# Kernel optimization log

Measured on AMD Instinct MI355X. Metric: run time of the kernel, lower is better.

## Reference

```python
import jax, jax.numpy as jnp
import numpy as np

EPS = 1e-6
NUM_HEADS = 16

def _ln(x):
    m = jnp.mean(x, -1, keepdims=True)
    v = jnp.mean((x - m) ** 2, -1, keepdims=True)
    return (x - m) * jax.lax.rsqrt(v + EPS)

def _rms(x, w):
    return x * jax.lax.rsqrt(jnp.mean(x * x, -1, keepdims=True) + EPS) * w

def _to_mha(t):
    B, S, D = t.shape
    return t.reshape(B, S, NUM_HEADS, D // NUM_HEADS).transpose(0, 2, 1, 3)

def _rope(t, freqs):
    # t: [B,H,T,Hd], freqs: [T, Hd//2, 2] (cos, sin)
    B, H, T, Hd = t.shape
    tr = t.reshape(B, H, T, Hd // 2, 2)
    cos, sin = freqs[..., 0], freqs[..., 1]
    r = tr[..., 0] * cos - tr[..., 1] * sin
    i = tr[..., 0] * sin + tr[..., 1] * cos
    return jnp.stack([r, i], -1).reshape(B, H, T, Hd)

def _pre(h, qk_w, qn, kn, v_w, v_b):
    qk = h @ qk_w.T                      # [B,S,2D], no bias (c_qk bias=False)
    q, k = jnp.split(qk, 2, -1)
    q = _rms(_to_mha(q), qn)             # per-head RMSNorm
    k = _rms(_to_mha(k), kn)
    v = _to_mha(h @ v_w.T + v_b)
    return q, k, v

def _post(x, a, pw, pb, w1, b1, w3, b3, w2, b2):
    x = x + a @ pw.T + pb                # residual + c_proj
    h = _ln(x)
    m = (jax.nn.silu(h @ w1.T + b1) * (h @ w3.T + b3)) @ w2.T + b2  # SwiGLU
    return x + m

def _forward(x, c, freqs, px_qk_w, px_qn, px_kn, px_v_w, px_v_b,
             pc_qk_w, pc_qn, pc_kn, pc_v_w, pc_v_b,
             p1_proj_w, p1_proj_b, p1_w1, p1_b1, p1_w3, p1_b3, p1_w2, p1_b2,
             p2_proj_w, p2_proj_b, p2_w1, p2_b1, p2_w3, p2_b3, p2_w2, p2_b2):
    x_ln, c_ln = _ln(x), _ln(c)
    qc, kc, vc = _pre(c_ln, pc_qk_w, pc_qn, pc_kn, pc_v_w, pc_v_b)
    qx, kx, vx = _pre(x_ln, px_qk_w, px_qn, px_kn, px_v_w, px_v_b)
    q = jnp.concatenate([qc, qx], 2)     # [B,H,T,Hd], T = S+L
    k = jnp.concatenate([kc, kx], 2)
    v = jnp.concatenate([vc, vx], 2)
    q = _rope(q, freqs)
    k = _rope(k, freqs)
    Hd = q.shape[-1]
    scores = jnp.einsum('bhqd,bhkd->bhqk', q, k) / jnp.sqrt(jnp.float32(Hd))
    T = scores.shape[-1]
    causal = jnp.tril(jnp.ones((T, T), bool))
    scores = jnp.where(causal, scores, jnp.finfo(scores.dtype).min)
    p = jax.nn.softmax(scores, -1)
    y = jnp.einsum('bhqk,bhkd->bhqd', p, v)
    B, D = x.shape[0], x.shape[-1]
    y = y.transpose(0, 2, 1, 3).reshape(B, -1, D)  # [B,T,D]
    S = c.shape[1]
    y_c, y_x = y[:, :S], y[:, S:]
    x_out = _post(x, y_x, p1_proj_w, p1_proj_b, p1_w1, p1_b1, p1_w3, p1_b3, p1_w2, p1_b2)
    c_out = _post(c, y_c, p2_proj_w, p2_proj_b, p2_w1, p2_b1, p2_w3, p2_b3, p2_w2, p2_b2)
    return x_out, c_out

def setup_inputs() -> dict:
    B, L, S, D, H, FF = 1, 1536, 512, 1024, 16, 4096
    Hd, T = D // H, L + S
    key = jax.random.key(0)
    ks = iter(jax.random.split(key, 40))
    def rn(shape, s=0.02):
        return (jax.random.normal(next(ks), shape, jnp.float32) * s)
    pos = jnp.arange(T, dtype=jnp.float32)
    inv = 1.0 / (10000.0 ** (jnp.arange(0, Hd, 2, dtype=jnp.float32) / Hd))
    ang = pos[:, None] * inv[None, :]
    freqs = jnp.stack([jnp.cos(ang), jnp.sin(ang)], -1)  # [T, Hd//2, 2]
    inp = {
        'x': jax.random.normal(next(ks), (B, L, D), jnp.float32),
        'c': jax.random.normal(next(ks), (B, S, D), jnp.float32),
        'freqs': freqs,
        'px_qk_w': rn((2 * D, D)), 'px_qn': jnp.ones((Hd,)), 'px_kn': jnp.ones((Hd,)),
        'px_v_w': rn((D, D)), 'px_v_b': rn((D,)),
        'pc_qk_w': rn((2 * D, D)), 'pc_qn': jnp.ones((Hd,)), 'pc_kn': jnp.ones((Hd,)),
        'pc_v_w': rn((D, D)), 'pc_v_b': rn((D,)),
    }
    for pfx in ('p1', 'p2'):
        inp[pfx + '_proj_w'] = rn((D, D)); inp[pfx + '_proj_b'] = rn((D,))
        inp[pfx + '_w1'] = rn((FF, D)); inp[pfx + '_b1'] = rn((FF,))
        inp[pfx + '_w3'] = rn((FF, D)); inp[pfx + '_b3'] = rn((FF,))
        inp[pfx + '_w2'] = rn((D, FF)); inp[pfx + '_b2'] = rn((D,))
    return inp

def reference(x, c, freqs, px_qk_w, px_qn, px_kn, px_v_w, px_v_b,
              pc_qk_w, pc_qn, pc_kn, pc_v_w, pc_v_b,
              p1_proj_w, p1_proj_b, p1_w1, p1_b1, p1_w3, p1_b3, p1_w2, p1_b2,
              p2_proj_w, p2_proj_b, p2_w1, p2_b1, p2_w3, p2_b3, p2_w2, p2_b2):
    return _forward(x, c, freqs, px_qk_w, px_qn, px_kn, px_v_w, px_v_b,
                    pc_qk_w, pc_qn, pc_kn, pc_v_w, pc_v_b,
                    p1_proj_w, p1_proj_b, p1_w1, p1_b1, p1_w3, p1_b3, p1_w2, p1_b2,
                    p2_proj_w, p2_proj_b, p2_w1, p2_b1, p2_w3, p2_b3, p2_w2, p2_b2)
```

## Files before the change

kernel.cpp:

```cpp
#include <hip/hip_runtime.h>

typedef __attribute__((ext_vector_type(8))) short short8;
typedef __attribute__((ext_vector_type(4))) float floatx4;

__device__ __forceinline__ float bf2f(unsigned short u) {
  union { unsigned int i; float f; } v; v.i = ((unsigned int)u) << 16; return v.f;
}
__device__ __forceinline__ unsigned short f2bf(float f) {
  union { float f; unsigned int i; } v; v.f = f;
  unsigned int x = v.i + 0x7fffu + ((v.i >> 16) & 1u);
  return (unsigned short)(x >> 16);
}
__device__ __forceinline__ float loadE(const void* p, size_t i, int f) {
  return f ? ((const float*)p)[i] : bf2f(((const unsigned short*)p)[i]);
}
__device__ __forceinline__ uint4 packbf(float4 a, float4 b) {
  union { unsigned short u[8]; uint4 v; } p;
  p.u[0] = f2bf(a.x); p.u[1] = f2bf(a.y); p.u[2] = f2bf(a.z); p.u[3] = f2bf(a.w);
  p.u[4] = f2bf(b.x); p.u[5] = f2bf(b.y); p.u[6] = f2bf(b.z); p.u[7] = f2bf(b.w);
  return p.v;
}

__device__ __forceinline__ void gl16(const unsigned short* g, unsigned short* l) {
  __builtin_amdgcn_global_load_lds(
      (const __attribute__((address_space(1))) void*)g,
      (__attribute__((address_space(3))) void*)l, 16, 0, 0);
}

__global__ void detect_kernel(const unsigned int* __restrict__ probe, int* __restrict__ flag) {
  if (threadIdx.x == 0 && blockIdx.x == 0) *flag = (probe[0] == 0x3F800000u) ? 1 : 0;
}

struct CArgs {
  const void* in[12];
  unsigned short* out[12];
  unsigned int cum[12];
};
__global__ __launch_bounds__(256) void convw_kernel(CArgs a, int total_chunks,
                                                    const int* __restrict__ flagp) {
  const int flag = *flagp;
  for (int c = blockIdx.x * 256 + threadIdx.x; c < total_chunks; c += gridDim.x * 256) {
    int s = 0;
    while (c >= (int)a.cum[s]) ++s;
    unsigned int base = s ? a.cum[s - 1] : 0u;
    size_t e = (size_t)(c - base) * 8;
    if (flag) {
      const float* in = (const float*)a.in[s] + e;
      float4 v0 = *(const float4*)in;
      float4 v1 = *(const float4*)(in + 4);
      *(uint4*)(a.out[s] + e) = packbf(v0, v1);
    } else {
      *(uint4*)(a.out[s] + e) = *(const uint4*)((const unsigned short*)a.in[s] + e);
    }
  }
}

__global__ __launch_bounds__(256) void zero_kernel(void* __restrict__ out, int out_elems,
                                                   const int* __restrict__ flagp) {
  int limit = (*flagp) ? (out_elems >> 2) : (out_elems >> 3);
  int i = blockIdx.x * 256 + threadIdx.x;
  if (i < limit) ((uint4*)out)[i] = make_uint4(0, 0, 0, 0);
}

__global__ __launch_bounds__(256) void reduce_kernel(const float* __restrict__ part,
                                                     const unsigned short* __restrict__ mid,
                                                     const void* __restrict__ b1,
                                                     const void* __restrict__ b2,
                                                     float* __restrict__ out,
                                                     const int* __restrict__ flagp) {
  if (!*flagp) return;
  const size_t TD = 2097152, LD = (size_t)1536 * 1024, SD = (size_t)512 * 1024;
  size_t i = ((size_t)blockIdx.x * 256 + threadIdx.x) * 4;
  if (i >= TD) return;
  float4 v  = *(const float4*)(part + i);
  float4 v1 = *(const float4*)(part + TD + i);
  float4 v2 = *(const float4*)(part + 2 * TD + i);
  float4 v3 = *(const float4*)(part + 3 * TD + i);
  v.x += v1.x + v2.x + v3.x;
  v.y += v1.y + v2.y + v3.y;
  v.z += v1.z + v2.z + v3.z;
  v.w += v1.w + v2.w + v3.w;
  int col = (int)(i & 1023);
  const float* bias = (const float*)((i < LD) ? b1 : b2);
  size_t ri = (i < LD) ? (SD + i) : (i - LD);
  v.x += bias[col + 0] + bf2f(mid[ri + 0]);
  v.y += bias[col + 1] + bf2f(mid[ri + 1]);
  v.z += bias[col + 2] + bf2f(mid[ri + 2]);
  v.w += bias[col + 3] + bf2f(mid[ri + 3]);
  *(float4*)(out + i) = v;
}

__global__ __launch_bounds__(256) void ln_ext_kernel(const void* __restrict__ cin,
                                                     const void* __restrict__ xin,
                                                     unsigned short* __restrict__ out,
                                                     const int* __restrict__ flagp) {
  const int D = 1024, S = 512;
  const int flag = *flagp;
  int row = blockIdx.x;
  const void* src = (row < S) ? cin : xin;
  size_t rb = (size_t)(row < S ? row : row - S) * D;
  int base = threadIdx.x * 4;
  float x0 = loadE(src, rb + base + 0, flag);
  float x1 = loadE(src, rb + base + 1, flag);
  float x2 = loadE(src, rb + base + 2, flag);
  float x3 = loadE(src, rb + base + 3, flag);
  float s1 = x0 + x1 + x2 + x3;
  float s2 = x0 * x0 + x1 * x1 + x2 * x2 + x3 * x3;
  for (int off = 32; off; off >>= 1) {
    s1 += __shfl_down(s1, off, 64);
    s2 += __shfl_down(s2, off, 64);
  }
  __shared__ float red[8];
  int wid = threadIdx.x >> 6;
  if ((threadIdx.x & 63) == 0) { red[wid] = s1; red[4 + wid] = s2; }
  __syncthreads();
  s1 = red[0] + red[1] + red[2] + red[3];
  s2 = red[4] + red[5] + red[6] + red[7];
  float mean = s1 * (1.0f / D);
  float var = s2 * (1.0f / D) - mean * mean;
  float inv = rsqrtf(var + 1e-6f);
  unsigned short* dst = out + (size_t)row * D + base;
  dst[0] = f2bf((x0 - mean) * inv);
  dst[1] = f2bf((x1 - mean) * inv);
  dst[2] = f2bf((x2 - mean) * inv);
  dst[3] = f2bf((x3 - mean) * inv);
}

__global__ __launch_bounds__(256) void ln_mid_kernel(const unsigned short* __restrict__ in,
                                                     unsigned short* __restrict__ outc,
                                                     unsigned short* __restrict__ outx) {
  const int D = 1024, S = 512;
  int row = blockIdx.x;
  const unsigned short* src = in + (size_t)row * D;
  int base = threadIdx.x * 4;
  float x0 = bf2f(src[base + 0]);
  float x1 = bf2f(src[base + 1]);
  float x2 = bf2f(src[base + 2]);
  float x3 = bf2f(src[base + 3]);
  float s1 = x0 + x1 + x2 + x3;
  float s2 = x0 * x0 + x1 * x1 + x2 * x2 + x3 * x3;
  for (int off = 32; off; off >>= 1) {
    s1 += __shfl_down(s1, off, 64);
    s2 += __shfl_down(s2, off, 64);
  }
  __shared__ float red[8];
  int wid = threadIdx.x >> 6;
  if ((threadIdx.x & 63) == 0) { red[wid] = s1; red[4 + wid] = s2; }
  __syncthreads();
  s1 = red[0] + red[1] + red[2] + red[3];
  s2 = red[4] + red[5] + red[6] + red[7];
  float mean = s1 * (1.0f / D);
  float var = s2 * (1.0f / D) - mean * mean;
  float inv = rsqrtf(var + 1e-6f);
  unsigned short* dst = (row < S ? outc + (size_t)row * D : outx + (size_t)(row - S) * D) + base;
  dst[0] = f2bf((x0 - mean) * inv);
  dst[1] = f2bf((x1 - mean) * inv);
  dst[2] = f2bf((x2 - mean) * inv);
  dst[3] = f2bf((x3 - mean) * inv);
}

struct GArgs {
  const unsigned short* A[4];
  const void* B[4];
  const void* bias[4];
  const void* res[4];
  void* C[4];
  unsigned long long oo[4];
  int mcum[4];
  int N[4];
  int K;
  int nd;
  float* part;
};

#define BAR() asm volatile("s_waitcnt lgkmcnt(0)\n\ts_barrier" ::: "memory")
#define FBAR() asm volatile("s_waitcnt vmcnt(0) lgkmcnt(0)\n\ts_barrier" ::: "memory")

template <int RES_MODE, int OUT_MODE, int SPLITK, int BBF16>
__global__ __launch_bounds__(256) void gemm_kernel(GArgs g, const int* __restrict__ flagp) {
  const int flag = *flagp;
  int by = blockIdx.y;
  int d = 0;
  while (d < g.nd - 1 && by >= g.mcum[d]) ++d;
  int mbase = (d == 0) ? 0 : g.mcum[d - 1];
  const int m0 = (by - mbase) * 128;
  const int N = g.N[d];
  const int n0 = blockIdx.x * 128;
  if (n0 >= N) return;
  const int K = g.K;
  int kbeg = 0, kend = K;
  if (SPLITK > 1) {
    if (!flag) {
      if (blockIdx.z != 0) return;
    } else {
      int kl = K / SPLITK;
      kbeg = blockIdx.z * kl;
      kend = kbeg + kl;
    }
  }
  const int nt = (kend - kbeg) >> 5;

  constexpr int BSTRIDE = BBF16 ? 4096 : 5120;
  __shared__ __align__(16) unsigned short sA[2 * BSTRIDE];
  __shared__ __align__(16) unsigned short sB[2 * BSTRIDE];

  const int tid = threadIdx.x;
  const int lane = tid & 63;
  const int wave = tid >> 6;
  const int wm = (wave >> 1) * 64, wn = (wave & 1) * 64;
  const int srow = tid >> 2;
  const int scol = BBF16 ? ((((tid & 3) ^ ((tid >> 3) & 3))) * 8) : ((tid & 3) * 8);
  const unsigned short* Ag0 = g.A[d] + (size_t)(m0 + srow) * K + kbeg + scol;
  const unsigned short* Ag1 = Ag0 + (size_t)64 * K;
  const unsigned short* Bh0 = (const unsigned short*)g.B[d] + (size_t)(n0 + srow) * K + kbeg + scol;
  const unsigned short* Bh1 = Bh0 + (size_t)64 * K;

  const int fr = lane & 15;
  const int rdo = BBF16 ? ((((lane >> 4) ^ ((fr >> 1) & 3))) * 8) : ((lane >> 4) * 8);
  constexpr int PITCH = BBF16 ? 32 : 40;
  floatx4 acc[4][4] = {};
  auto compute = [&](const unsigned short* as, const unsigned short* bs) {
    short8 af[4], bfr[4];
    #pragma unroll
    for (int i = 0; i < 4; ++i) {
      af[i]  = *(const short8*)(as + (wm + i * 16 + fr) * PITCH + rdo);
      bfr[i] = *(const short8*)(bs + (wn + i * 16 + fr) * PITCH + rdo);
    }
    #pragma unroll
    for (int mi = 0; mi < 4; ++mi)
      #pragma unroll
      for (int ni = 0; ni < 4; ++ni)
        acc[mi][ni] = __builtin_amdgcn_mfma_f32_16x16x32_bf16(af[mi], bfr[ni], acc[mi][ni], 0, 0, 0);
  };

  if (BBF16) {
    unsigned short* lA0 = sA + wave * 512;
    unsigned short* lA1 = lA0 + 2048;
    unsigned short* lB0 = sB + wave * 512;
    unsigned short* lB1 = lB0 + 2048;
    auto stage = [&](int buf, int kk) {
      int bo = buf * 4096;
      gl16(Ag0 + kk, lA0 + bo);
      gl16(Ag1 + kk, lA1 + bo);
      gl16(Bh0 + kk, lB0 + bo);
      gl16(Bh1 + kk, lB1 + bo);
    };
    stage(0, 0);
    FBAR();
    for (int t = 0; t < nt; ++t) {
      if (t + 1 < nt) stage((t + 1) & 1, (t + 1) * 32);
      compute(sA + (t & 1) * 4096, sB + (t & 1) * 4096);
      if (t + 1 < nt) FBAR();
    }
  } else {
    const float* Bf0 = (const float*)g.B[d] + (size_t)(n0 + srow) * K + kbeg + scol;
    const float* Bf1 = Bf0 + (size_t)64 * K;
    const int wo0 = srow * 40 + scol;
    const int wo1 = wo0 + 64 * 40;
    uint4 ra0, ra1, rb0, rb1;
    auto load_tile = [&](int kk) {
      ra0 = *(const uint4*)(Ag0 + kk);
      ra1 = *(const uint4*)(Ag1 + kk);
      if (!flag) {
        rb0 = *(const uint4*)(Bh0 + kk);
        rb1 = *(const uint4*)(Bh1 + kk);
      } else {
        float4 x0 = *(const float4*)(Bf0 + kk), x1 = *(const float4*)(Bf0 + kk + 4);
        float4 y0 = *(const float4*)(Bf1 + kk), y1 = *(const float4*)(Bf1 + kk + 4);
        rb0 = packbf(x0, x1);
        rb1 = packbf(y0, y1);
      }
    };
    auto store_tile = [&](int buf) {
      unsigned short* sa = sA + buf * 5120;
      unsigned short* sb = sB + buf * 5120;
      *(uint4*)(sa + wo0) = ra0;
      *(uint4*)(sa + wo1) = ra1;
      *(uint4*)(sb + wo0) = rb0;
      *(uint4*)(sb + wo1) = rb1;
    };
    load_tile(0);
    store_tile(0);
    if (nt > 1) load_tile(32);
    BAR();
    for (int t = 0; t < nt; ++t) {
      if (t + 1 < nt) {
        store_tile((t + 1) & 1);
        if (t + 2 < nt) load_tile((t + 2) * 32);
      }
      compute(sA + (t & 1) * 5120, sB + (t & 1) * 5120);
      if (t + 1 < nt) BAR();
    }
  }

  const void* bias = g.bias[d];
  const void* res = g.res[d];
  void* C = g.C[d];
  const size_t oo = g.oo[d];
  const bool first = (SPLITK <= 1) || (blockIdx.z == 0) || !flag;
  const bool rawpart = (OUT_MODE == 3) && (flag != 0);
  #pragma unroll
  for (int mi = 0; mi < 4; ++mi)
    #pragma unroll
    for (int ni = 0; ni < 4; ++ni)
      #pragma unroll
      for (int r = 0; r < 4; ++r) {
        int row = m0 + wm + mi * 16 + (lane >> 4) * 4 + r;
        int col = n0 + wn + ni * 16 + (lane & 15);
        float val = acc[mi][ni][r];
        size_t off = (size_t)row * N + col;
        if (first && !rawpart) {
          if (bias) val += loadE(bias, (size_t)col, flag);
          if (RES_MODE == 1) val += loadE(res, off, flag);
          if (RES_MODE == 3) {
            float h1v = bf2f(((const unsigned short*)res)[off]);
            val = (h1v / (1.0f + __expf(-h1v))) * val;
          }
          if (RES_MODE == 4) val += bf2f(((const unsigned short*)res)[off]);
        }
        if (OUT_MODE == 0) {
          ((unsigned short*)C)[off] = f2bf(val);
        } else if (OUT_MODE == 3) {
          if (flag) g.part[(size_t)blockIdx.z * 2097152 + oo + off] = val;
          else      ((unsigned short*)C)[oo + off] = f2bf(val);
        } else {
          if (flag) {
            if (SPLITK > 1) atomicAdd((float*)C + oo + off, val);
            else            ((float*)C)[oo + off] = val;
          } else {
            ((unsigned short*)C)[oo + off] = f2bf(val);
          }
        }
      }
}

__global__ __launch_bounds__(256) void rmsrope_kernel(
    unsigned short* __restrict__ qk,
    const void* __restrict__ qn_c, const void* __restrict__ kn_c,
    const void* __restrict__ qn_x, const void* __restrict__ kn_x,
    const void* __restrict__ freqs, const int* __restrict__ flagp) {
  const int flag = *flagp;
  int t = blockIdx.x;
  int h = blockIdx.y * 4 + (threadIdx.x >> 6);
  int d = threadIdx.x & 63;
  unsigned short* qrow = qk + (size_t)t * 2048 + h * 64;
  unsigned short* krow = qrow + 1024;
  float q = bf2f(qrow[d]), k = bf2f(krow[d]);
  float qs = q * q, ks = k * k;
  for (int off = 32; off; off >>= 1) {
    qs += __shfl_xor(qs, off, 64);
    ks += __shfl_xor(ks, off, 64);
  }
  const void* qn = (t < 512) ? qn_c : qn_x;
  const void* kn = (t < 512) ? kn_c : kn_x;
  q = q * rsqrtf(qs * (1.0f / 64.0f) + 1e-6f) * loadE(qn, d, flag);
  k = k * rsqrtf(ks * (1.0f / 64.0f) + 1e-6f) * loadE(kn, d, flag);
  int j = d >> 1;
  float cv = loadE(freqs, (size_t)(t * 32 + j) * 2 + 0, flag);
  float sv = loadE(freqs, (size_t)(t * 32 + j) * 2 + 1, flag);
  float qo = __shfl_xor(q, 1, 64);
  float ko = __shfl_xor(k, 1, 64);
  float qn2, kn2;
  if ((d & 1) == 0) { qn2 = q * cv - qo * sv; kn2 = k * cv - ko * sv; }
  else              { qn2 = qo * sv + q * cv; kn2 = ko * sv + k * cv; }
  qrow[d] = f2bf(qn2);
  krow[d] = f2bf(kn2);
}

__global__ __launch_bounds__(256) void attn_kernel(const unsigned short* __restrict__ qk,
                                                   const unsigned short* __restrict__ v,
                                                   unsigned short* __restrict__ y) {
  int id = blockIdx.x;
  int blk = (id & 256) ? (31 - (id & 31)) : (id & 31);
  int h = (id >> 5) & 15;
  int wv = threadIdx.x >> 6;
  int lane = threadIdx.x & 63;
  int qbase = blk * 64 + wv * 16;

  __shared__ __align__(16) unsigned short Ks[64 * 72];
  __shared__ __align__(16) unsigned short Vt[64 * 64];
  __shared__ __align__(16) unsigned short ps[4][16 * 72];

  short8 qa[2];
  {
    int m = lane & 15, dj = (lane >> 4) * 8;
    const unsigned short* qp = qk + (size_t)(qbase + m) * 2048 + h * 64 + dj;
    qa[0] = *(const short8*)(qp);
    qa[1] = *(const short8*)(qp + 32);
  }
  floatx4 o[4] = {};
  float mrow[4] = {-1e30f, -1e30f, -1e30f, -1e30f};
  float lrow[4] = {0.f, 0.f, 0.f, 0.f};
  int ntiles = blk + 1;
  for (int tile = 0; tile < ntiles; ++tile) {
    int j0 = tile * 64;
    __syncthreads();
    for (int c2 = threadIdx.x; c2 < 512; c2 += 256) {
      int key = c2 >> 3, d0 = (c2 & 7) * 8;
      *(short8*)(Ks + key * 72 + d0) =
          *(const short8*)(qk + (size_t)(j0 + key) * 2048 + 1024 + h * 64 + d0);
      short8 vv = *(const short8*)(v + (size_t)(j0 + key) * 1024 + h * 64 + d0);
      int bphys = ((key >> 3) ^ (d0 >> 3)) * 8 + (key & 7);
      #pragma unroll
      for (int jj = 0; jj < 8; ++jj)
        Vt[(d0 + jj) * 64 + bphys] = ((const unsigned short*)&vv)[jj];
    }
    __syncthreads();
    floatx4 sacc[4];
    #pragma unroll
    for (int kg = 0; kg < 4; ++kg) {
      floatx4 z = {0.f, 0.f, 0.f, 0.f};
      #pragma unroll
      for (int kc = 0; kc < 2; ++kc) {
        short8 kb = *(const short8*)(Ks + (kg * 16 + (lane & 15)) * 72 + kc * 32 + (lane >> 4) * 8);
        z = __builtin_amdgcn_mfma_f32_16x16x32_bf16(qa[kc], kb, z, 0, 0, 0);
      }
      sacc[kg] = z;
    }
    #pragma unroll
    for (int kg = 0; kg < 4; ++kg)
      #pragma unroll
      for (int r = 0; r < 4; ++r) {
        int key_g = j0 + kg * 16 + (lane & 15);
        int q_g = qbase + (lane >> 4) * 4 + r;
        float s = sacc[kg][r] * 0.125f;
        sacc[kg][r] = (key_g <= q_g) ? s : -1e30f;
      }
    #pragma unroll
    for (int r = 0; r < 4; ++r) {
      float mx = fmaxf(fmaxf(sacc[0][r], sacc[1][r]), fmaxf(sacc[2][r], sacc[3][r]));
      mx = fmaxf(mx, __shfl_xor(mx, 1, 64));
      mx = fmaxf(mx, __shfl_xor(mx, 2, 64));
      mx = fmaxf(mx, __shfl_xor(mx, 4, 64));
      mx = fmaxf(mx, __shfl_xor(mx, 8, 64));
      float mnew = fmaxf(mrow[r], mx);
      float al = __expf(mrow[r] - mnew);
      mrow[r] = mnew;
      float sum = 0.f;
      #pragma unroll
      for (int kg = 0; kg < 4; ++kg) {
        float p = __expf(sacc[kg][r] - mnew);
        sacc[kg][r] = p;
        sum += p;
      }
      sum += __shfl_xor(sum, 1, 64);
      sum += __shfl_xor(sum, 2, 64);
      sum += __shfl_xor(sum, 4, 64);
      sum += __shfl_xor(sum, 8, 64);
      lrow[r] = lrow[r] * al + sum;
      #pragma unroll
      for (int ni = 0; ni < 4; ++ni) o[ni][r] *= al;
    }
    unsigned short* pw = ps[wv];
    #pragma unroll
    for (int kg = 0; kg < 4; ++kg)
      #pragma unroll
      for (int r = 0; r < 4; ++r)
        pw[((lane >> 4) * 4 + r) * 72 + kg * 16 + (lane & 15)] = f2bf(sacc[kg][r]);
    asm volatile("s_waitcnt lgkmcnt(0)" ::: "memory");
    short8 pa[2];
    pa[0] = *(const short8*)(pw + (lane & 15) * 72 + (lane >> 4) * 8);
    pa[1] = *(const short8*)(pw + (lane & 15) * 72 + 32 + (lane >> 4) * 8);
    #pragma unroll
    for (int ni = 0; ni < 4; ++ni) {
      floatx4 z = o[ni];
      int dd = ni * 16 + (lane & 15);
      #pragma unroll
      for (int kc = 0; kc < 2; ++kc) {
        int bphys = (kc * 4 + (lane >> 4)) ^ (dd >> 3);
        short8 vb = *(const short8*)(Vt + dd * 64 + bphys * 8);
        z = __builtin_amdgcn_mfma_f32_16x16x32_bf16(pa[kc], vb, z, 0, 0, 0);
      }
      o[ni] = z;
    }
  }
  #pragma unroll
  for (int ni = 0; ni < 4; ++ni)
    #pragma unroll
    for (int r = 0; r < 4; ++r) {
      int q = qbase + (lane >> 4) * 4 + r;
      int dd = ni * 16 + (lane & 15);
      y[(size_t)q * 1024 + h * 64 + dd] = f2bf(o[ni][r] / lrow[r]);
    }
}

extern "C" void kernel_launch(void* const* d_in, const int* in_sizes, int n_in,
                              void* d_out, int out_size, void* d_ws, size_t ws_size,
                              hipStream_t stream) {
  const int L = 1536, S = 512, D = 1024, T = 2048, FF = 4096;
  const void* x        = d_in[0];
  const void* c        = d_in[1];
  const void* freqs    = d_in[2];
  const void* px_qk_w  = d_in[3];
  const void* px_qn    = d_in[4];
  const void* px_kn    = d_in[5];
  const void* px_v_w   = d_in[6];
  const void* px_v_b   = d_in[7];
  const void* pc_qk_w  = d_in[8];
  const void* pc_qn    = d_in[9];
  const void* pc_kn    = d_in[10];
  const void* pc_v_w   = d_in[11];
  const void* pc_v_b   = d_in[12];
  const void* p1_proj_w = d_in[13];
  const void* p1_proj_b = d_in[14];
  const void* p1_w1 = d_in[15];
  const void* p1_b1 = d_in[16];
  const void* p1_w3 = d_in[17];
  const void* p1_b3 = d_in[18];
  const void* p1_w2 = d_in[19];
  const void* p1_b2 = d_in[20];
  const void* p2_proj_w = d_in[21];
  const void* p2_proj_b = d_in[22];
  const void* p2_w1 = d_in[23];
  const void* p2_b1 = d_in[24];
  const void* p2_w3 = d_in[25];
  const void* p2_b3 = d_in[26];
  const void* p2_w2 = d_in[27];
  const void* p2_b2 = d_in[28];

  char* ws = (char*)d_ws;
  unsigned short* hln     = (unsigned short*)(ws);
  unsigned short* ybuf    = (unsigned short*)(ws);
  unsigned short* h1c     = (unsigned short*)(ws);
  unsigned short* qkbuf   = (unsigned short*)(ws + ((size_t)4  << 20));
  unsigned short* h1x     = (unsigned short*)(ws + ((size_t)4  << 20));
  unsigned short* vbuf    = (unsigned short*)(ws + ((size_t)12 << 20));
  unsigned short* mid     = (unsigned short*)(ws + ((size_t)16 << 20));
  unsigned short* midln_c = (unsigned short*)(ws + ((size_t)20 << 20));
  int*            flag    = (int*)(ws + ((size_t)21 << 20));
  unsigned short* midln_x = (unsigned short*)d_out;
  unsigned short* hlnx    = hln + (size_t)S * D;

  const bool conv = ws_size >= ((size_t)90 << 20);
  unsigned short* wbf = (unsigned short*)(ws + ((size_t)24 << 20));
  unsigned short* b_qk_c = wbf + 0;
  unsigned short* b_qk_x = wbf + 2097152;
  unsigned short* b_v_c  = wbf + 4194304;
  unsigned short* b_v_x  = wbf + 5242880;
  unsigned short* b_pj1  = wbf + 6291456;
  unsigned short* b_pj2  = wbf + 7340032;
  unsigned short* b_w1p1 = wbf + 8388608;
  unsigned short* b_w1p2 = wbf + 12582912;
  unsigned short* b_w3p1 = wbf + 16777216;
  unsigned short* b_w3p2 = wbf + 20971520;
  unsigned short* b_w2p1 = wbf + 25165824;
  unsigned short* b_w2p2 = wbf + 29360128;
  float* part = (float*)(ws + ((size_t)40 << 20));

  detect_kernel<<<1, 64, 0, stream>>>((const unsigned int*)px_qn, flag);

  if (conv) {
    CArgs ca;
    const void* ins[12]   = {pc_qk_w, px_qk_w, pc_v_w, px_v_w, p1_proj_w, p2_proj_w,
                             p1_w1, p2_w1, p1_w3, p2_w3, p1_w2, p2_w2};
    unsigned short* os[12] = {b_qk_c, b_qk_x, b_v_c, b_v_x, b_pj1, b_pj2,
                              b_w1p1, b_w1p2, b_w3p1, b_w3p2, b_w2p1, b_w2p2};
    unsigned int cnt[12]  = {262144, 262144, 131072, 131072, 131072, 131072,
                             524288, 524288, 524288, 524288, 524288, 524288};
    unsigned int cum = 0;
    for (int i = 0; i < 12; ++i) { ca.in[i] = ins[i]; ca.out[i] = os[i]; cum += cnt[i]; ca.cum[i] = cum; }
    convw_kernel<<<2048, 256, 0, stream>>>(ca, (int)cum, flag);
  }

  ln_ext_kernel<<<T, 256, 0, stream>>>(c, x, hln, flag);

  {
    GArgs g = {};
    g.A[0] = hln;  g.bias[0] = nullptr; g.C[0] = qkbuf;                    g.mcum[0] = 4;  g.N[0] = 2048;
    g.A[1] = hlnx; g.bias[1] = nullptr; g.C[1] = qkbuf + (size_t)S * 2048; g.mcum[1] = 16; g.N[1] = 2048;
    g.A[2] = hln;  g.bias[2] = pc_v_b;  g.C[2] = vbuf;                     g.mcum[2] = 20; g.N[2] = 1024;
    g.A[3] = hlnx; g.bias[3] = px_v_b;  g.C[3] = vbuf + (size_t)S * D;     g.mcum[3] = 32; g.N[3] = 1024;
    g.K = 1024; g.nd = 4;
    if (conv) {
      g.B[0] = b_qk_c; g.B[1] = b_qk_x; g.B[2] = b_v_c; g.B[3] = b_v_x;
      gemm_kernel<0, 0, 1, 1><<<dim3(16, 32), 256, 0, stream>>>(g, flag);
    } else {
      g.B[0] = pc_qk_w; g.B[1] = px_qk_w; g.B[2] = pc_v_w; g.B[3] = px_v_w;
      gemm_kernel<0, 0, 1, 0><<<dim3(16, 32), 256, 0, stream>>>(g, flag);
    }
  }
  rmsrope_kernel<<<dim3(T, 4), 256, 0, stream>>>(qkbuf, pc_qn, pc_kn, px_qn, px_kn, freqs, flag);
  attn_kernel<<<512, 256, 0, stream>>>(qkbuf, vbuf, ybuf);

  {
    GArgs g = {};
    g.A[0] = ybuf;                  g.bias[0] = p2_proj_b; g.res[0] = c; g.C[0] = mid;                  g.mcum[0] = 4;  g.N[0] = 1024;
    g.A[1] = ybuf + (size_t)S * D;  g.bias[1] = p1_proj_b; g.res[1] = x; g.C[1] = mid + (size_t)S * D;  g.mcum[1] = 16; g.N[1] = 1024;
    g.K = 1024; g.nd = 2;
    if (conv) {
      g.B[0] = b_pj2; g.B[1] = b_pj1;
      gemm_kernel<1, 0, 1, 1><<<dim3(8, 16), 256, 0, stream>>>(g, flag);
    } else {
      g.B[0] = p2_proj_w; g.B[1] = p1_proj_w;
      gemm_kernel<1, 0, 1, 0><<<dim3(8, 16), 256, 0, stream>>>(g, flag);
    }
  }
  ln_mid_kernel<<<T, 256, 0, stream>>>(mid, midln_c, midln_x);

  {
    GArgs g = {};
    g.A[0] = midln_x; g.bias[0] = p1_b1; g.C[0] = h1x; g.mcum[0] = 12; g.N[0] = 4096;
    g.A[1] = midln_c; g.bias[1] = p2_b1; g.C[1] = h1c; g.mcum[1] = 16; g.N[1] = 4096;
    g.K = 1024; g.nd = 2;
    if (conv) {
      g.B[0] = b_w1p1; g.B[1] = b_w1p2;
      gemm_kernel<0, 0, 1, 1><<<dim3(32, 16), 256, 0, stream>>>(g, flag);
    } else {
      g.B[0] = p1_w1; g.B[1] = p2_w1;
      gemm_kernel<0, 0, 1, 0><<<dim3(32, 16), 256, 0, stream>>>(g, flag);
    }
  }
  {
    GArgs g = {};
    g.A[0] = midln_x; g.bias[0] = p1_b3; g.res[0] = h1x; g.C[0] = h1x; g.mcum[0] = 12; g.N[0] = 4096;
    g.A[1] = midln_c; g.bias[1] = p2_b3; g.res[1] = h1c; g.C[1] = h1c; g.mcum[1] = 16; g.N[1] = 4096;
    g.K = 1024; g.nd = 2;
    if (conv) {
      g.B[0] = b_w3p1; g.B[1] = b_w3p2;
      gemm_kernel<3, 0, 1, 1><<<dim3(32, 16), 256, 0, stream>>>(g, flag);
    } else {
      g.B[0] = p1_w3; g.B[1] = p2_w3;
      gemm_kernel<3, 0, 1, 0><<<dim3(32, 16), 256, 0, stream>>>(g, flag);
    }
  }
  if (conv) {
    GArgs g = {};
    g.A[0] = h1x; g.bias[0] = p1_b2; g.res[0] = mid + (size_t)S * D; g.C[0] = d_out; g.oo[0] = 0;             g.mcum[0] = 12; g.N[0] = 1024;
    g.A[1] = h1c; g.bias[1] = p2_b2; g.res[1] = mid;                 g.C[1] = d_out; g.oo[1] = (size_t)L * D; g.mcum[1] = 16; g.N[1] = 1024;
    g.K = 4096; g.nd = 2;
    g.part = part;
    g.B[0] = b_w2p1; g.B[1] = b_w2p2;
    gemm_kernel<4, 3, 4, 1><<<dim3(8, 16, 4), 256, 0, stream>>>(g, flag);
    reduce_kernel<<<2048, 256, 0, stream>>>(part, mid, p1_b2, p2_b2, (float*)d_out, flag);
  } else {
    zero_kernel<<<2048, 256, 0, stream>>>(d_out, out_size, flag);
    GArgs g = {};
    g.A[0] = h1x; g.bias[0] = p1_b2; g.res[0] = mid + (size_t)S * D; g.C[0] = d_out; g.oo[0] = 0;             g.mcum[0] = 12; g.N[0] = 1024;
    g.A[1] = h1c; g.bias[1] = p2_b2; g.res[1] = mid;                 g.C[1] = d_out; g.oo[1] = (size_t)L * D; g.mcum[1] = 16; g.N[1] = 1024;
    g.K = 4096; g.nd = 2;
    g.B[0] = p1_w2; g.B[1] = p2_w2;
    gemm_kernel<4, 2, 4, 0><<<dim3(8, 16, 4), 256, 0, stream>>>(g, flag);
  }
}
```

Before: 511.8 us.

## Write V transposed from GEMM epilogue and double-buffer attention K/V via async LDS loads

The QKV GEMM epilogue now writes the V projection transposed ([D, T] layout) with 4-wide packed stores. This lets the attention kernel load V tiles directly instead of transposing them element by element into shared memory. The attention kernel now uses global_load_lds to stage K and V into double-buffered, XOR-swizzled LDS tiles, prefetching the next tile while the current one is computed. The costs are strided transposed stores in the GEMM epilogue and twice the LDS footprint in attention, which may lower occupancy.

```diff
diff --git a/kernel.cpp b/kernel.cpp
--- a/kernel.cpp
+++ b/kernel.cpp
@@ -2,6 +2,7 @@
 
 typedef __attribute__((ext_vector_type(8))) short short8;
 typedef __attribute__((ext_vector_type(4))) float floatx4;
+typedef __attribute__((ext_vector_type(4))) unsigned short ushortx4;
 
 __device__ __forceinline__ float bf2f(unsigned short u) {
   union { unsigned int i; float f; } v; v.i = ((unsigned int)u) << 16; return v.f;
@@ -170,6 +171,7 @@
   int N[4];
   int K;
   int nd;
+  int tmask;
   float* part;
 };
 
@@ -299,39 +301,54 @@
   const size_t oo = g.oo[d];
   const bool first = (SPLITK <= 1) || (blockIdx.z == 0) || !flag;
   const bool rawpart = (OUT_MODE == 3) && (flag != 0);
+  const bool trans = (OUT_MODE == 0) && (((g.tmask) >> d) & 1);
   #pragma unroll
   for (int mi = 0; mi < 4; ++mi)
     #pragma unroll
-    for (int ni = 0; ni < 4; ++ni)
-      #pragma unroll
-      for (int r = 0; r < 4; ++r) {
-        int row = m0 + wm + mi * 16 + (lane >> 4) * 4 + r;
-        int col = n0 + wn + ni * 16 + (lane & 15);
-        float val = acc[mi][ni][r];
-        size_t off = (size_t)row * N + col;
-        if (first && !rawpart) {
-          if (bias) val += loadE(bias, (size_t)col, flag);
-          if (RES_MODE == 1) val += loadE(res, off, flag);
-          if (RES_MODE == 3) {
-            float h1v = bf2f(((const unsigned short*)res)[off]);
-            val = (h1v / (1.0f + __expf(-h1v))) * val;
+    for (int ni = 0; ni < 4; ++ni) {
+      int colb = n0 + wn + ni * 16 + (lane & 15);
+      int rowb = m0 + wm + mi * 16 + (lane >> 4) * 4;
+      if (trans) {
+        ushortx4 o4;
+        #pragma unroll
+        for (int r = 0; r < 4; ++r) {
+          float val = acc[mi][ni][r];
+          if (bias) val += loadE(bias, (size_t)colb, flag);
+          o4[r] = f2bf(val);
+        }
+        *(ushortx4*)((unsigned short*)C + (size_t)colb * 2048 + oo + rowb) = o4;
+      } else {
+        #pragma unroll
+        for (int r = 0; r < 4; ++r) {
+          int row = rowb + r;
+          int col = colb;
+          float val = acc[mi][ni][r];
+          size_t off = (size_t)row * N + col;
+          if (first && !rawpart) {
+            if (bias) val += loadE(bias, (size_t)col, flag);
+            if (RES_MODE == 1) val += loadE(res, off, flag);
+            if (RES_MODE == 3) {
+              float h1v = bf2f(((const unsigned short*)res)[off]);
+              val = (h1v / (1.0f + __expf(-h1v))) * val;
+            }
+            if (RES_MODE == 4) val += bf2f(((const unsigned short*)res)[off]);
           }
-          if (RES_MODE == 4) val += bf2f(((const unsigned short*)res)[off]);
-        }
-        if (OUT_MODE == 0) {
-          ((unsigned short*)C)[off] = f2bf(val);
-        } else if (OUT_MODE == 3) {
-          if (flag) g.part[(size_t)blockIdx.z * 2097152 + oo + off] = val;
-          else      ((unsigned short*)C)[oo + off] = f2bf(val);
-        } else {
-          if (flag) {
-            if (SPLITK > 1) atomicAdd((float*)C + oo + off, val);
-            else            ((float*)C)[oo + off] = val;
+          if (OUT_MODE == 0) {
+            ((unsigned short*)C)[off] = f2bf(val);
+          } else if (OUT_MODE == 3) {
+            if (flag) g.part[(size_t)blockIdx.z * 2097152 + oo + off] = val;
+            else      ((unsigned short*)C)[oo + off] = f2bf(val);
           } else {
-            ((unsigned short*)C)[oo + off] = f2bf(val);
+            if (flag) {
+              if (SPLITK > 1) atomicAdd((float*)C + oo + off, val);
+              else            ((float*)C)[oo + off] = val;
+            } else {
+              ((unsigned short*)C)[oo + off] = f2bf(val);
+            }
           }
         }
       }
+    }
 }
 
 __global__ __launch_bounds__(256) void rmsrope_kernel(
@@ -368,7 +385,7 @@
 }
 
 __global__ __launch_bounds__(256) void attn_kernel(const unsigned short* __restrict__ qk,
-                                                   const unsigned short* __restrict__ v,
+                                                   const unsigned short* __restrict__ vT,
                                                    unsigned short* __restrict__ y) {
   int id = blockIdx.x;
   int blk = (id & 256) ? (31 - (id & 31)) : (id & 31);
@@ -377,9 +394,28 @@
   int lane = threadIdx.x & 63;
   int qbase = blk * 64 + wv * 16;
 
-  __shared__ __align__(16) unsigned short Ks[64 * 72];
-  __shared__ __align__(16) unsigned short Vt[64 * 64];
+  __shared__ __align__(16) unsigned short Ks[2 * 4096];
+  __shared__ __align__(16) unsigned short Vs[2 * 4096];
   __shared__ __align__(16) unsigned short ps[4][16 * 72];
+
+  const int c0 = wv * 64 + lane;
+  const int r0 = c0 >> 3,         k0 = (c0 & 7) ^ (r0 & 7);
+  const int r1 = (c0 + 256) >> 3, k1 = (c0 & 7) ^ (r1 & 7);
+  unsigned short* kd0 = Ks + wv * 512;
+  unsigned short* kd1 = Ks + 2048 + wv * 512;
+  unsigned short* vd0 = Vs + wv * 512;
+  unsigned short* vd1 = Vs + 2048 + wv * 512;
+  const unsigned short* kgp0 = qk + 1024 + h * 64 + k0 * 8 + (size_t)r0 * 2048;
+  const unsigned short* kgp1 = qk + 1024 + h * 64 + k1 * 8 + (size_t)r1 * 2048;
+  const unsigned short* vgp0 = vT + (size_t)(h * 64 + r0) * 2048 + k0 * 8;
+  const unsigned short* vgp1 = vT + (size_t)(h * 64 + r1) * 2048 + k1 * 8;
+  auto stage = [&](int buf, int j0) {
+    int bo = buf * 4096;
+    gl16(kgp0 + (size_t)j0 * 2048, kd0 + bo);
+    gl16(kgp1 + (size_t)j0 * 2048, kd1 + bo);
+    gl16(vgp0 + j0, vd0 + bo);
+    gl16(vgp1 + j0, vd1 + bo);
+  };
 
   short8 qa[2];
   {
@@ -392,27 +428,23 @@
   float mrow[4] = {-1e30f, -1e30f, -1e30f, -1e30f};
   float lrow[4] = {0.f, 0.f, 0.f, 0.f};
   int ntiles = blk + 1;
+
+  stage(0, 0);
+  FBAR();
   for (int tile = 0; tile < ntiles; ++tile) {
     int j0 = tile * 64;
-    __syncthreads();
-    for (int c2 = threadIdx.x; c2 < 512; c2 += 256) {
-      int key = c2 >> 3, d0 = (c2 & 7) * 8;
-      *(short8*)(Ks + key * 72 + d0) =
-          *(const short8*)(qk + (size_t)(j0 + key) * 2048 + 1024 + h * 64 + d0);
-      short8 vv = *(const short8*)(v + (size_t)(j0 + key) * 1024 + h * 64 + d0);
-      int bphys = ((key >> 3) ^ (d0 >> 3)) * 8 + (key & 7);
-      #pragma unroll
-      for (int jj = 0; jj < 8; ++jj)
-        Vt[(d0 + jj) * 64 + bphys] = ((const unsigned short*)&vv)[jj];
-    }
-    __syncthreads();
+    if (tile + 1 < ntiles) stage((tile + 1) & 1, j0 + 64);
+    const unsigned short* Kb = Ks + (tile & 1) * 4096;
+    const unsigned short* Vb = Vs + (tile & 1) * 4096;
     floatx4 sacc[4];
     #pragma unroll
     for (int kg = 0; kg < 4; ++kg) {
       floatx4 z = {0.f, 0.f, 0.f, 0.f};
       #pragma unroll
       for (int kc = 0; kc < 2; ++kc) {
-        short8 kb = *(const short8*)(Ks + (kg * 16 + (lane & 15)) * 72 + kc * 32 + (lane >> 4) * 8);
+        int kr = kg * 16 + (lane & 15);
+        int p = (kc * 4 + (lane >> 4)) ^ (kr & 7);
+        short8 kb = *(const short8*)(Kb + kr * 64 + p * 8);
         z = __builtin_amdgcn_mfma_f32_16x16x32_bf16(qa[kc], kb, z, 0, 0, 0);
       }
       sacc[kg] = z;
@@ -467,12 +499,13 @@
       int dd = ni * 16 + (lane & 15);
       #pragma unroll
       for (int kc = 0; kc < 2; ++kc) {
-        int bphys = (kc * 4 + (lane >> 4)) ^ (dd >> 3);
-        short8 vb = *(const short8*)(Vt + dd * 64 + bphys * 8);
+        int p = (kc * 4 + (lane >> 4)) ^ (dd & 7);
+        short8 vb = *(const short8*)(Vb + dd * 64 + p * 8);
         z = __builtin_amdgcn_mfma_f32_16x16x32_bf16(pa[kc], vb, z, 0, 0, 0);
       }
       o[ni] = z;
     }
+    if (tile + 1 < ntiles) FBAR();
   }
   #pragma unroll
   for (int ni = 0; ni < 4; ++ni)
@@ -524,7 +557,7 @@
   unsigned short* h1c     = (unsigned short*)(ws);
   unsigned short* qkbuf   = (unsigned short*)(ws + ((size_t)4  << 20));
   unsigned short* h1x     = (unsigned short*)(ws + ((size_t)4  << 20));
-  unsigned short* vbuf    = (unsigned short*)(ws + ((size_t)12 << 20));
+  unsigned short* vbufT   = (unsigned short*)(ws + ((size_t)12 << 20));
   unsigned short* mid     = (unsigned short*)(ws + ((size_t)16 << 20));
   unsigned short* midln_c = (unsigned short*)(ws + ((size_t)20 << 20));
   int*            flag    = (int*)(ws + ((size_t)21 << 20));
@@ -568,9 +601,9 @@
     GArgs g = {};
     g.A[0] = hln;  g.bias[0] = nullptr; g.C[0] = qkbuf;                    g.mcum[0] = 4;  g.N[0] = 2048;
     g.A[1] = hlnx; g.bias[1] = nullptr; g.C[1] = qkbuf + (size_t)S * 2048; g.mcum[1] = 16; g.N[1] = 2048;
-    g.A[2] = hln;  g.bias[2] = pc_v_b;  g.C[2] = vbuf;                     g.mcum[2] = 20; g.N[2] = 1024;
-    g.A[3] = hlnx; g.bias[3] = px_v_b;  g.C[3] = vbuf + (size_t)S * D;     g.mcum[3] = 32; g.N[3] = 1024;
-    g.K = 1024; g.nd = 4;
+    g.A[2] = hln;  g.bias[2] = pc_v_b;  g.C[2] = vbufT; g.oo[2] = 0;       g.mcum[2] = 20; g.N[2] = 1024;
+    g.A[3] = hlnx; g.bias[3] = px_v_b;  g.C[3] = vbufT; g.oo[3] = S;       g.mcum[3] = 32; g.N[3] = 1024;
+    g.K = 1024; g.nd = 4; g.tmask = 0b1100;
     if (conv) {
       g.B[0] = b_qk_c; g.B[1] = b_qk_x; g.B[2] = b_v_c; g.B[3] = b_v_x;
       gemm_kernel<0, 0, 1, 1><<<dim3(16, 32), 256, 0, stream>>>(g, flag);
@@ -580,7 +613,7 @@
     }
   }
   rmsrope_kernel<<<dim3(T, 4), 256, 0, stream>>>(qkbuf, pc_qn, pc_kn, px_qn, px_kn, freqs, flag);
-  attn_kernel<<<512, 256, 0, stream>>>(qkbuf, vbuf, ybuf);
+  attn_kernel<<<512, 256, 0, stream>>>(qkbuf, vbufT, ybuf);
 
   {
     GArgs g = {};
```

New measurement: 500.6 us. -2.2%, faster.
